# Kernel optimization log

Hardware: AMD Instinct MI355X
Metric: run time of the kernel (lower is better)

The kernel has to match this reference:

```python
import jax, jax.numpy as jnp
import numpy as np

# --- static Cayley table for Cl(3) (8 blades) ---
def _derive_cayley_table():
    basis_gens = [(), (1,), (2,), (3,), (1, 2), (1, 3), (2, 3), (1, 2, 3)]
    gens_to_idx = {g: i for i, g in enumerate(basis_gens)}
    def reduce(a, b):
        gens = list(a) + list(b)
        sign = 1
        changed = True
        while changed:
            changed = False
            i = 0
            while i < len(gens) - 1:
                if gens[i] == gens[i + 1]:
                    gens.pop(i); gens.pop(i)
                    changed = True
                    if i > 0:
                        i -= 1
                elif gens[i] > gens[i + 1]:
                    gens[i], gens[i + 1] = gens[i + 1], gens[i]
                    sign *= -1
                    changed = True
                    i += 1
                else:
                    i += 1
        return gens_to_idx[tuple(gens)], sign
    return [[reduce(basis_gens[i], basis_gens[j]) for j in range(8)] for i in range(8)]

_TAB = _derive_cayley_table()
SI = np.array([i for i in range(8) for _ in range(8)], dtype=np.int32)
SJ = np.array([j for _ in range(8) for j in range(8)], dtype=np.int32)
TK = np.array([_TAB[i][j][0] for i in range(8) for j in range(8)], dtype=np.int32)
SG = np.array([float(_TAB[i][j][1]) for i in range(8) for j in range(8)], dtype=np.float32)

N_TOK, N_BLADE, D_BLADE, D_FFN = 8192, 8, 256, 1024
LN_EPS = 1e-5


def setup_inputs() -> dict:
    key = jax.random.key(0)
    ks = jax.random.split(key, 5)
    scale = 0.02
    return {
        'x': jax.random.normal(ks[0], (N_TOK, N_BLADE, D_BLADE), jnp.float32),
        'interaction_weights': jnp.full((64,), 0.1, jnp.float32),
        'geo_gate': jnp.asarray(0.5, jnp.float32),
        'ln_w': jnp.ones((D_BLADE,), jnp.float32),
        'ln_b': jnp.zeros((D_BLADE,), jnp.float32),
        'W_gate': jax.random.normal(ks[1], (D_BLADE, D_FFN), jnp.float32) * scale,
        'W_up': jax.random.normal(ks[2], (D_BLADE, D_FFN), jnp.float32) * scale,
        'W_down': jax.random.normal(ks[3], (D_FFN, D_BLADE), jnp.float32) * scale,
    }


def reference(x, interaction_weights, geo_gate, ln_w, ln_b, W_gate, W_up, W_down):
    si = jnp.asarray(SI); sj = jnp.asarray(SJ); tk = jnp.asarray(TK)
    sg = jnp.asarray(SG).astype(x.dtype)
    w = jax.nn.sigmoid(interaction_weights).astype(x.dtype)
    # gather blade pairs, weighted Cayley product: (N, 64, D)
    products = x[:, si, :] * x[:, sj, :] * (sg * w)[None, :, None]
    # scatter-add into target blades: (N, 8, D)
    geo = jnp.zeros_like(x).at[:, tk, :].add(products)
    g = jax.nn.sigmoid(geo_gate)
    mixed = g * geo + (1.0 - g) * x
    # LayerNorm over D
    flat = mixed.reshape(-1, x.shape[-1])
    mu = jnp.mean(flat, axis=-1, keepdims=True)
    var = jnp.var(flat, axis=-1, keepdims=True)
    flat = (flat - mu) * jax.lax.rsqrt(var + LN_EPS) * ln_w + ln_b
    # SwiGLU FFN
    h = jax.nn.silu(flat @ W_gate) * (flat @ W_up)
    out = (h @ W_down).reshape(x.shape)
    return x + out
```

## Files before the change

### kernel.cpp

```cpp
#include <hip/hip_runtime.h>
#include <hip/hip_bf16.h>

typedef __bf16 bf16x8 __attribute__((ext_vector_type(8)));
typedef float floatx4 __attribute__((ext_vector_type(4)));

constexpr int TK[64] = {
  0,1,2,3,4,5,6,7,
  1,0,4,5,2,3,7,6,
  2,4,0,6,1,7,3,5,
  3,5,6,0,7,1,2,4,
  4,2,1,7,0,6,5,3,
  5,3,7,1,6,0,4,2,
  6,7,3,2,5,4,0,1,
  7,6,5,4,3,2,1,0
};
constexpr float SGN[64] = {
  1, 1, 1, 1, 1, 1, 1, 1,
  1, 1, 1, 1, 1, 1, 1, 1,
  1,-1, 1, 1,-1,-1, 1,-1,
  1,-1,-1, 1, 1,-1,-1, 1,
  1,-1, 1, 1,-1,-1, 1,-1,
  1,-1,-1, 1, 1,-1,-1, 1,
  1, 1,-1, 1,-1, 1,-1,-1,
  1, 1,-1, 1,-1, 1,-1,-1
};

__device__ __forceinline__ void async16(const void* g, void* l) {
  __builtin_amdgcn_global_load_lds(
      (const __attribute__((address_space(1))) void*)g,
      (__attribute__((address_space(3))) void*)l, 16, 0, 0);
}

__global__ __launch_bounds__(256) void conv_w(
    const float* __restrict__ Wg, const float* __restrict__ Wu, const float* __restrict__ Wd,
    __bf16* __restrict__ Bg, __bf16* __restrict__ Bu, __bf16* __restrict__ Bd)
{
  int idx = blockIdx.x * 256 + threadIdx.x;
  {
    int n = idx >> 8, k = idx & 255;
    Bg[idx] = (__bf16)Wg[k * 1024 + n];
    Bu[idx] = (__bf16)Wu[k * 1024 + n];
  }
  {
    int n = idx >> 10, k = idx & 1023;
    Bd[idx] = (__bf16)Wd[k * 256 + n];
  }
}

__global__ __launch_bounds__(256) void geo_ln(
    const float* __restrict__ X,
    const float* __restrict__ IW,
    const float* __restrict__ GG,
    const float* __restrict__ LW, const float* __restrict__ LB,
    __bf16* __restrict__ F)
{
  __shared__ float sw[64];
  __shared__ float smix[8 * 256];
  __shared__ float sstat[16];
  const int t = threadIdx.x;
  const int tok = blockIdx.x;

  if (t < 64) sw[t] = SGN[t] / (1.f + __expf(-IW[t]));

  float xv[8];
  #pragma unroll
  for (int b = 0; b < 8; ++b) xv[b] = X[(size_t)tok * 2048 + b * 256 + t];
  const float g = 1.f / (1.f + __expf(-GG[0]));

  __syncthreads();

  float geo[8] = {0.f, 0.f, 0.f, 0.f, 0.f, 0.f, 0.f, 0.f};
  #pragma unroll
  for (int p = 0; p < 64; ++p)
    geo[TK[p]] += xv[p >> 3] * xv[p & 7] * sw[p];

  float mv[8];
  #pragma unroll
  for (int b = 0; b < 8; ++b) {
    mv[b] = g * geo[b] + (1.f - g) * xv[b];
    smix[b * 256 + t] = mv[b];
  }
  __syncthreads();

  const int wv = t >> 6, lane = t & 63;
  #pragma unroll
  for (int s = 0; s < 2; ++s) {
    int b = wv * 2 + s;
    float v0 = smix[b * 256 + lane];
    float v1 = smix[b * 256 + 64 + lane];
    float v2 = smix[b * 256 + 128 + lane];
    float v3 = smix[b * 256 + 192 + lane];
    float sum = v0 + v1 + v2 + v3;
    float sq  = v0*v0 + v1*v1 + v2*v2 + v3*v3;
    #pragma unroll
    for (int off = 32; off > 0; off >>= 1) {
      sum += __shfl_xor(sum, off, 64);
      sq  += __shfl_xor(sq,  off, 64);
    }
    if (lane == 0) {
      float mu  = sum * (1.f / 256.f);
      float var = sq * (1.f / 256.f) - mu * mu;
      sstat[b]     = mu;
      sstat[8 + b] = rsqrtf(var + 1e-5f);
    }
  }
  __syncthreads();

  const float lw = LW[t], lb = LB[t];
  #pragma unroll
  for (int b = 0; b < 8; ++b) {
    float v = (mv[b] - sstat[b]) * sstat[8 + b] * lw + lb;
    F[(size_t)(tok * 8 + b) * 256 + t] = (__bf16)v;
  }
}

__global__ __launch_bounds__(256) void gemm_gateup(
    const __bf16* __restrict__ A,
    const __bf16* __restrict__ Bg,
    const __bf16* __restrict__ Bu,
    __bf16* __restrict__ H)
{
  __shared__ __bf16 sA[128 * 32];
  __shared__ __bf16 sBg[64 * 32];
  __shared__ __bf16 sBu[64 * 32];
  const int t = threadIdx.x;
  const int m0 = blockIdx.x * 128;
  const int f0 = blockIdx.y * 64;
  const int lane = t & 63, wv = t >> 6;
  const int wm = wv & 1, wf = wv >> 1;
  const int l15 = lane & 15, quad = lane >> 4;

  floatx4 zero = {0.f, 0.f, 0.f, 0.f};
  floatx4 accg[4][2], accu[4][2];
  #pragma unroll
  for (int im = 0; im < 4; ++im)
    #pragma unroll
    for (int jf = 0; jf < 2; ++jf) { accg[im][jf] = zero; accu[im][jf] = zero; }

  for (int k0 = 0; k0 < 256; k0 += 32) {
    #pragma unroll
    for (int i = 0; i < 2; ++i) {
      int idx = i * 256 + t;
      int row = idx >> 2, seg = idx & 3;
      async16(A + (size_t)(m0 + row) * 256 + k0 + seg * 8, &sA[idx * 8]);
    }
    {
      int row = t >> 2, seg = t & 3;
      async16(Bg + (size_t)(f0 + row) * 256 + k0 + seg * 8, &sBg[t * 8]);
      async16(Bu + (size_t)(f0 + row) * 256 + k0 + seg * 8, &sBu[t * 8]);
    }
    __syncthreads();

    bf16x8 af[4], bgf[2], buf[2];
    #pragma unroll
    for (int im = 0; im < 4; ++im)
      af[im] = *(const bf16x8*)&sA[(wm * 64 + im * 16 + l15) * 32 + quad * 8];
    #pragma unroll
    for (int jf = 0; jf < 2; ++jf) {
      bgf[jf] = *(const bf16x8*)&sBg[(wf * 32 + jf * 16 + l15) * 32 + quad * 8];
      buf[jf] = *(const bf16x8*)&sBu[(wf * 32 + jf * 16 + l15) * 32 + quad * 8];
    }
    #pragma unroll
    for (int im = 0; im < 4; ++im)
      #pragma unroll
      for (int jf = 0; jf < 2; ++jf) {
        accg[im][jf] = __builtin_amdgcn_mfma_f32_16x16x32_bf16(af[im], bgf[jf], accg[im][jf], 0, 0, 0);
        accu[im][jf] = __builtin_amdgcn_mfma_f32_16x16x32_bf16(af[im], buf[jf], accu[im][jf], 0, 0, 0);
      }
    __syncthreads();
  }

  #pragma unroll
  for (int im = 0; im < 4; ++im)
    #pragma unroll
    for (int jf = 0; jf < 2; ++jf)
      #pragma unroll
      for (int r = 0; r < 4; ++r) {
        int m = m0 + wm * 64 + im * 16 + quad * 4 + r;
        int f = f0 + wf * 32 + jf * 16 + l15;
        float gv = accg[im][jf][r];
        float uv = accu[im][jf][r];
        float hv = (gv / (1.f + __expf(-gv))) * uv;
        H[(size_t)m * 1024 + f] = (__bf16)hv;
      }
}

__global__ __launch_bounds__(256) void gemm_down(
    const __bf16* __restrict__ A,
    const __bf16* __restrict__ B,
    const float* __restrict__ X,
    float* __restrict__ O)
{
  __shared__ __bf16 sA[128 * 32];
  __shared__ __bf16 sB[256 * 32];
  const int t = threadIdx.x;
  const int m0 = blockIdx.x * 128;
  const int lane = t & 63, wv = t >> 6;
  const int wm = wv & 1, wn = wv >> 1;
  const int l15 = lane & 15, quad = lane >> 4;

  floatx4 zero = {0.f, 0.f, 0.f, 0.f};
  floatx4 acc[4][8];
  #pragma unroll
  for (int im = 0; im < 4; ++im)
    #pragma unroll
    for (int jn = 0; jn < 8; ++jn) acc[im][jn] = zero;

  for (int k0 = 0; k0 < 1024; k0 += 32) {
    #pragma unroll
    for (int i = 0; i < 2; ++i) {
      int idx = i * 256 + t, row = idx >> 2, seg = idx & 3;
      async16(A + (size_t)(m0 + row) * 1024 + k0 + seg * 8, &sA[idx * 8]);
    }
    #pragma unroll
    for (int i = 0; i < 4; ++i) {
      int idx = i * 256 + t, row = idx >> 2, seg = idx & 3;
      async16(B + (size_t)row * 1024 + k0 + seg * 8, &sB[idx * 8]);
    }
    __syncthreads();

    bf16x8 af[4], bfr[8];
    #pragma unroll
    for (int im = 0; im < 4; ++im)
      af[im] = *(const bf16x8*)&sA[(wm * 64 + im * 16 + l15) * 32 + quad * 8];
    #pragma unroll
    for (int jn = 0; jn < 8; ++jn)
      bfr[jn] = *(const bf16x8*)&sB[(wn * 128 + jn * 16 + l15) * 32 + quad * 8];
    #pragma unroll
    for (int im = 0; im < 4; ++im)
      #pragma unroll
      for (int jn = 0; jn < 8; ++jn)
        acc[im][jn] = __builtin_amdgcn_mfma_f32_16x16x32_bf16(af[im], bfr[jn], acc[im][jn], 0, 0, 0);
    __syncthreads();
  }

  #pragma unroll
  for (int im = 0; im < 4; ++im)
    #pragma unroll
    for (int jn = 0; jn < 8; ++jn)
      #pragma unroll
      for (int r = 0; r < 4; ++r) {
        int m = m0 + wm * 64 + im * 16 + quad * 4 + r;
        int n = wn * 128 + jn * 16 + l15;
        size_t o = (size_t)m * 256 + n;
        O[o] = X[o] + acc[im][jn][r];
      }
}

extern "C" void kernel_launch(void* const* d_in, const int* in_sizes, int n_in,
                              void* d_out, int out_size, void* d_ws, size_t ws_size,
                              hipStream_t stream) {
  const float* x   = (const float*)d_in[0];
  const float* iw  = (const float*)d_in[1];
  const float* gg  = (const float*)d_in[2];
  const float* lnw = (const float*)d_in[3];
  const float* lnb = (const float*)d_in[4];
  const float* Wg  = (const float*)d_in[5];
  const float* Wu  = (const float*)d_in[6];
  const float* Wd  = (const float*)d_in[7];
  float* out = (float*)d_out;

  char* ws = (char*)d_ws;
  __bf16* flat = (__bf16*)(ws);
  __bf16* h    = (__bf16*)(ws + 33554432);
  __bf16* Bg   = (__bf16*)(ws + 167772160);
  __bf16* Bu   = (__bf16*)(ws + 168296448);
  __bf16* Bd   = (__bf16*)(ws + 168820736);

  conv_w<<<1024, 256, 0, stream>>>(Wg, Wu, Wd, Bg, Bu, Bd);
  geo_ln<<<8192, 256, 0, stream>>>(x, iw, gg, lnw, lnb, flat);
  gemm_gateup<<<dim3(512, 16), 256, 0, stream>>>(flat, Bg, Bu, h);
  gemm_down<<<512, 256, 0, stream>>>(h, Bd, x, out);
}
```

Measured before the change: 328.7 us.

## Enlarge GEMM K-tiles to 64 with XOR-swizzled LDS and bigger gate/up M tile

```diff
diff --git a/kernel.cpp b/kernel.cpp
--- a/kernel.cpp
+++ b/kernel.cpp
@@ -114,136 +114,172 @@
   }
 }
 
-__global__ __launch_bounds__(256) void gemm_gateup(
+__global__ __launch_bounds__(256, 2) void gemm_gateup(
     const __bf16* __restrict__ A,
     const __bf16* __restrict__ Bg,
     const __bf16* __restrict__ Bu,
     __bf16* __restrict__ H)
 {
-  __shared__ __bf16 sA[128 * 32];
-  __shared__ __bf16 sBg[64 * 32];
-  __shared__ __bf16 sBu[64 * 32];
+  __shared__ __bf16 sA[256 * 64];
+  __shared__ __bf16 sBg[64 * 64];
+  __shared__ __bf16 sBu[64 * 64];
   const int t = threadIdx.x;
-  const int m0 = blockIdx.x * 128;
+  const int m0 = blockIdx.x * 256;
   const int f0 = blockIdx.y * 64;
   const int lane = t & 63, wv = t >> 6;
-  const int wm = wv & 1, wf = wv >> 1;
   const int l15 = lane & 15, quad = lane >> 4;
 
+  int aoff[8], boff[2];
+  #pragma unroll
+  for (int i = 0; i < 8; ++i) {
+    int idx = i * 256 + t, row = idx >> 3, slot = idx & 7;
+    int gseg = slot ^ (row & 7);
+    aoff[i] = (m0 + row) * 256 + gseg * 8;
+  }
+  #pragma unroll
+  for (int i = 0; i < 2; ++i) {
+    int idx = i * 256 + t, row = idx >> 3, slot = idx & 7;
+    int gseg = slot ^ (row & 7);
+    boff[i] = (f0 + row) * 256 + gseg * 8;
+  }
+
   floatx4 zero = {0.f, 0.f, 0.f, 0.f};
-  floatx4 accg[4][2], accu[4][2];
-  #pragma unroll
-  for (int im = 0; im < 4; ++im)
-    #pragma unroll
-    for (int jf = 0; jf < 2; ++jf) { accg[im][jf] = zero; accu[im][jf] = zero; }
-
-  for (int k0 = 0; k0 < 256; k0 += 32) {
+  floatx4 accg[4][4], accu[4][4];
+  #pragma unroll
+  for (int i = 0; i < 4; ++i)
+    #pragma unroll
+    for (int j = 0; j < 4; ++j) { accg[i][j] = zero; accu[i][j] = zero; }
+
+  const int xr = l15 & 7;
+  for (int k = 0; k < 4; ++k) {
+    const int kk = k * 64;
+    #pragma unroll
+    for (int i = 0; i < 8; ++i) async16(A + aoff[i] + kk, &sA[(i * 256 + t) * 8]);
     #pragma unroll
     for (int i = 0; i < 2; ++i) {
-      int idx = i * 256 + t;
-      int row = idx >> 2, seg = idx & 3;
-      async16(A + (size_t)(m0 + row) * 256 + k0 + seg * 8, &sA[idx * 8]);
-    }
-    {
-      int row = t >> 2, seg = t & 3;
-      async16(Bg + (size_t)(f0 + row) * 256 + k0 + seg * 8, &sBg[t * 8]);
-      async16(Bu + (size_t)(f0 + row) * 256 + k0 + seg * 8, &sBu[t * 8]);
+      async16(Bg + boff[i] + kk, &sBg[(i * 256 + t) * 8]);
+      async16(Bu + boff[i] + kk, &sBu[(i * 256 + t) * 8]);
     }
     __syncthreads();
 
-    bf16x8 af[4], bgf[2], buf[2];
-    #pragma unroll
-    for (int im = 0; im < 4; ++im)
-      af[im] = *(const bf16x8*)&sA[(wm * 64 + im * 16 + l15) * 32 + quad * 8];
-    #pragma unroll
-    for (int jf = 0; jf < 2; ++jf) {
-      bgf[jf] = *(const bf16x8*)&sBg[(wf * 32 + jf * 16 + l15) * 32 + quad * 8];
-      buf[jf] = *(const bf16x8*)&sBu[(wf * 32 + jf * 16 + l15) * 32 + quad * 8];
-    }
-    #pragma unroll
-    for (int im = 0; im < 4; ++im)
-      #pragma unroll
-      for (int jf = 0; jf < 2; ++jf) {
-        accg[im][jf] = __builtin_amdgcn_mfma_f32_16x16x32_bf16(af[im], bgf[jf], accg[im][jf], 0, 0, 0);
-        accu[im][jf] = __builtin_amdgcn_mfma_f32_16x16x32_bf16(af[im], buf[jf], accu[im][jf], 0, 0, 0);
-      }
+    #pragma unroll
+    for (int s = 0; s < 2; ++s) {
+      const int slot = (s * 4 + quad) ^ xr;
+      bf16x8 av[4], bg[4], bu[4];
+      #pragma unroll
+      for (int i = 0; i < 4; ++i) {
+        int r = wv * 64 + i * 16 + l15;
+        av[i] = *(const bf16x8*)&sA[r * 64 + slot * 8];
+      }
+      #pragma unroll
+      for (int j = 0; j < 4; ++j) {
+        int r = j * 16 + l15;
+        bg[j] = *(const bf16x8*)&sBg[r * 64 + slot * 8];
+        bu[j] = *(const bf16x8*)&sBu[r * 64 + slot * 8];
+      }
+      #pragma unroll
+      for (int i = 0; i < 4; ++i)
+        #pragma unroll
+        for (int j = 0; j < 4; ++j) {
+          accg[i][j] = __builtin_amdgcn_mfma_f32_16x16x32_bf16(av[i], bg[j], accg[i][j], 0, 0, 0);
+          accu[i][j] = __builtin_amdgcn_mfma_f32_16x16x32_bf16(av[i], bu[j], accu[i][j], 0, 0, 0);
+        }
+    }
     __syncthreads();
   }
 
   #pragma unroll
-  for (int im = 0; im < 4; ++im)
-    #pragma unroll
-    for (int jf = 0; jf < 2; ++jf)
+  for (int i = 0; i < 4; ++i)
+    #pragma unroll
+    for (int j = 0; j < 4; ++j)
       #pragma unroll
       for (int r = 0; r < 4; ++r) {
-        int m = m0 + wm * 64 + im * 16 + quad * 4 + r;
-        int f = f0 + wf * 32 + jf * 16 + l15;
-        float gv = accg[im][jf][r];
-        float uv = accu[im][jf][r];
+        int m = m0 + wv * 64 + i * 16 + quad * 4 + r;
+        int f = f0 + j * 16 + l15;
+        float gv = accg[i][j][r];
+        float uv = accu[i][j][r];
         float hv = (gv / (1.f + __expf(-gv))) * uv;
         H[(size_t)m * 1024 + f] = (__bf16)hv;
       }
 }
 
-__global__ __launch_bounds__(256) void gemm_down(
+__global__ __launch_bounds__(256, 2) void gemm_down(
     const __bf16* __restrict__ A,
     const __bf16* __restrict__ B,
     const float* __restrict__ X,
     float* __restrict__ O)
 {
-  __shared__ __bf16 sA[128 * 32];
-  __shared__ __bf16 sB[256 * 32];
+  __shared__ __bf16 sA[128 * 64];
+  __shared__ __bf16 sB[256 * 64];
   const int t = threadIdx.x;
   const int m0 = blockIdx.x * 128;
   const int lane = t & 63, wv = t >> 6;
   const int wm = wv & 1, wn = wv >> 1;
   const int l15 = lane & 15, quad = lane >> 4;
 
+  int aoff[4], boff[8];
+  #pragma unroll
+  for (int i = 0; i < 4; ++i) {
+    int idx = i * 256 + t, row = idx >> 3, slot = idx & 7;
+    int gseg = slot ^ (row & 7);
+    aoff[i] = (m0 + row) * 1024 + gseg * 8;
+  }
+  #pragma unroll
+  for (int i = 0; i < 8; ++i) {
+    int idx = i * 256 + t, row = idx >> 3, slot = idx & 7;
+    int gseg = slot ^ (row & 7);
+    boff[i] = row * 1024 + gseg * 8;
+  }
+
   floatx4 zero = {0.f, 0.f, 0.f, 0.f};
   floatx4 acc[4][8];
   #pragma unroll
-  for (int im = 0; im < 4; ++im)
-    #pragma unroll
-    for (int jn = 0; jn < 8; ++jn) acc[im][jn] = zero;
-
-  for (int k0 = 0; k0 < 1024; k0 += 32) {
-    #pragma unroll
-    for (int i = 0; i < 2; ++i) {
-      int idx = i * 256 + t, row = idx >> 2, seg = idx & 3;
-      async16(A + (size_t)(m0 + row) * 1024 + k0 + seg * 8, &sA[idx * 8]);
-    }
-    #pragma unroll
-    for (int i = 0; i < 4; ++i) {
-      int idx = i * 256 + t, row = idx >> 2, seg = idx & 3;
-      async16(B + (size_t)row * 1024 + k0 + seg * 8, &sB[idx * 8]);
-    }
+  for (int i = 0; i < 4; ++i)
+    #pragma unroll
+    for (int j = 0; j < 8; ++j) acc[i][j] = zero;
+
+  const int xr = l15 & 7;
+  for (int k = 0; k < 16; ++k) {
+    const int kk = k * 64;
+    #pragma unroll
+    for (int i = 0; i < 4; ++i) async16(A + aoff[i] + kk, &sA[(i * 256 + t) * 8]);
+    #pragma unroll
+    for (int i = 0; i < 8; ++i) async16(B + boff[i] + kk, &sB[(i * 256 + t) * 8]);
     __syncthreads();
 
-    bf16x8 af[4], bfr[8];
-    #pragma unroll
-    for (int im = 0; im < 4; ++im)
-      af[im] = *(const bf16x8*)&sA[(wm * 64 + im * 16 + l15) * 32 + quad * 8];
-    #pragma unroll
-    for (int jn = 0; jn < 8; ++jn)
-      bfr[jn] = *(const bf16x8*)&sB[(wn * 128 + jn * 16 + l15) * 32 + quad * 8];
-    #pragma unroll
-    for (int im = 0; im < 4; ++im)
-      #pragma unroll
-      for (int jn = 0; jn < 8; ++jn)
-        acc[im][jn] = __builtin_amdgcn_mfma_f32_16x16x32_bf16(af[im], bfr[jn], acc[im][jn], 0, 0, 0);
+    #pragma unroll
+    for (int s = 0; s < 2; ++s) {
+      const int slot = (s * 4 + quad) ^ xr;
+      bf16x8 av[4], bv[8];
+      #pragma unroll
+      for (int i = 0; i < 4; ++i) {
+        int r = wm * 64 + i * 16 + l15;
+        av[i] = *(const bf16x8*)&sA[r * 64 + slot * 8];
+      }
+      #pragma unroll
+      for (int j = 0; j < 8; ++j) {
+        int r = wn * 128 + j * 16 + l15;
+        bv[j] = *(const bf16x8*)&sB[r * 64 + slot * 8];
+      }
+      #pragma unroll
+      for (int i = 0; i < 4; ++i)
+        #pragma unroll
+        for (int j = 0; j < 8; ++j)
+          acc[i][j] = __builtin_amdgcn_mfma_f32_16x16x32_bf16(av[i], bv[j], acc[i][j], 0, 0, 0);
+    }
     __syncthreads();
   }
 
   #pragma unroll
-  for (int im = 0; im < 4; ++im)
-    #pragma unroll
-    for (int jn = 0; jn < 8; ++jn)
+  for (int i = 0; i < 4; ++i)
+    #pragma unroll
+    for (int j = 0; j < 8; ++j)
       #pragma unroll
       for (int r = 0; r < 4; ++r) {
-        int m = m0 + wm * 64 + im * 16 + quad * 4 + r;
-        int n = wn * 128 + jn * 16 + l15;
+        int m = m0 + wm * 64 + i * 16 + quad * 4 + r;
+        int n = wn * 128 + j * 16 + l15;
         size_t o = (size_t)m * 256 + n;
-        O[o] = X[o] + acc[im][jn][r];
+        O[o] = X[o] + acc[i][j][r];
       }
 }
 
@@ -269,6 +305,6 @@
 
   conv_w<<<1024, 256, 0, stream>>>(Wg, Wu, Wd, Bg, Bu, Bd);
   geo_ln<<<8192, 256, 0, stream>>>(x, iw, gg, lnw, lnb, flat);
-  gemm_gateup<<<dim3(512, 16), 256, 0, stream>>>(flat, Bg, Bu, h);
+  gemm_gateup<<<dim3(256, 16), 256, 0, stream>>>(flat, Bg, Bu, h);
   gemm_down<<<512, 256, 0, stream>>>(h, Bd, x, out);
 }
```

Result: slower. 352.0 us (+7.1%).
